# Kernel optimization log

Measured on AMD Instinct MI355X. Metric: run time of the kernel, lower is better.

Reference implementation:

```python
import math
import jax, jax.numpy as jnp
import numpy as np

B, T, C = 2, 2048, 1024
H, Ca = 16, 64


def setup_inputs() -> dict:
    key = jax.random.key(0)
    ks = jax.random.split(key, 5)
    # kaiming-uniform-ish scale for weights
    wb = 1.0 / math.sqrt(C)
    return {
        "x": jax.random.normal(ks[0], (B, T, C), dtype=jnp.float32),
        "w_q": jax.random.uniform(ks[1], (H, C, Ca), jnp.float32, -wb, wb),
        "w_k": jax.random.uniform(ks[2], (H, C, Ca), jnp.float32, -wb, wb),
        "w_v": jax.random.uniform(ks[3], (H, C, Ca), jnp.float32, -wb, wb),
        "w_o": jax.random.uniform(ks[4], (C, C), jnp.float32, -wb, wb),
    }


def reference(x, w_q, w_k, w_v, w_o):
    # x: [B,T,C]; w_q/w_k/w_v: [H,C,Ca]; w_o: [C,C]
    scale = 1.0 / math.sqrt(w_q.shape[-1])
    q = jnp.einsum("btc,hca->bhta", x, w_q)  # [B,H,T,Ca]
    k = jnp.einsum("btc,hca->bhta", x, w_k)
    v = jnp.einsum("btc,hca->bhta", x, w_v)
    s = jnp.einsum("bhta,bhsa->bhts", q, k)  # [B,H,T,T]
    # faithful to original: mask where tril(s)==0, scale applied after masking
    s_hat = jnp.where(jnp.tril(s) == 0, -jnp.inf, s * scale)
    a = jax.nn.softmax(s_hat, axis=-1)
    y = jnp.einsum("bhts,bhsa->bhta", a, v)  # [B,H,T,Ca]
    y_cat = y.transpose(0, 2, 1, 3).reshape(x.shape)  # [B,T,C]
    return y_cat @ w_o
```

## Files before the change

### kernel.cpp

```cpp
#include <hip/hip_runtime.h>
#include <stdint.h>

#define Bc 2
#define Tc 2048
#define Cn 1024
#define Hc 16
#define CAc 64

typedef __attribute__((ext_vector_type(8))) short short8;
typedef __attribute__((ext_vector_type(4))) float f32x4;

#define QSCALE 0.18033688011112042f

__device__ __forceinline__ unsigned short f2bf(float f) {
    unsigned int u = __builtin_bit_cast(unsigned int, f);
    return (unsigned short)((u + 0x7fffu + ((u >> 16) & 1u)) >> 16);
}
__device__ __forceinline__ unsigned int pack_rne(float a, float b) {
    return (unsigned int)f2bf(a) | ((unsigned int)f2bf(b) << 16);
}
__device__ __forceinline__ unsigned int pack_trunc(float a, float b) {
    return __builtin_amdgcn_perm(__builtin_bit_cast(unsigned int, b),
                                 __builtin_bit_cast(unsigned int, a), 0x07060302u);
}

__device__ __forceinline__ void async_cp16(const unsigned short* g, unsigned short* l) {
    __builtin_amdgcn_global_load_lds(
        (const __attribute__((address_space(1))) unsigned int*)g,
        (__attribute__((address_space(3))) unsigned int*)l,
        16, 0, 0);
}

__device__ __forceinline__ int detect_bf16(const unsigned short* x) {
    int c = 0;
#pragma unroll
    for (int i = 0; i < 64; i++) {
        unsigned short u = x[i * 2];
        int e = (u >> 7) & 0xFF;
        c += (e >= 0x68 && e <= 0x90);
    }
    return c > 32;
}

__device__ __forceinline__ unsigned short ld_elem(const void* base, size_t off, int isbf) {
    return isbf ? ((const unsigned short*)base)[off] : f2bf(((const float*)base)[off]);
}

__global__ __launch_bounds__(256) void prep(
    const void* __restrict__ xin, unsigned short* __restrict__ xb,
    const void* __restrict__ wq, const void* __restrict__ wk,
    const void* __restrict__ wv, const void* __restrict__ wo,
    unsigned short* __restrict__ wT, unsigned short* __restrict__ woT)
{
    const int isbf = detect_bf16((const unsigned short*)xin);
    const int bx = blockIdx.x;
    if (bx < 4096) {
        if (isbf) return;
        int idx = (bx * 256 + threadIdx.x) * 4;
        const float* xf = (const float*)xin;
        float4 v = *(const float4*)(xf + idx);
        uint2 p;
        p.x = pack_rne(v.x, v.y);
        p.y = pack_rne(v.z, v.w);
        *(uint2*)(&xb[idx]) = p;
        return;
    }
    __shared__ unsigned short tile[32][33];
    const int t = threadIdx.x;
    const int tx = t & 31, ty = t >> 5;
    const void* src;
    unsigned short* dst;
    int R, Cw, r0, c0;
    if (bx < 7168) {
        int rem0 = bx - 4096;
        int g = rem0 >> 6;
        int rem = rem0 & 63;
        int ct = rem >> 1;
        int at = rem & 1;
        int proj = g >> 4, h = g & 15;
        const void* wsel = (proj == 0) ? wq : ((proj == 1) ? wk : wv);
        src = isbf ? (const void*)((const unsigned short*)wsel + (size_t)h * Cn * CAc)
                   : (const void*)((const float*)wsel + (size_t)h * Cn * CAc);
        dst = wT + (size_t)g * CAc * Cn;
        R = Cn; Cw = CAc; r0 = ct * 32; c0 = at * 32;
    } else {
        int rem = bx - 7168;
        src = wo; dst = woT;
        R = Cn; Cw = Cn;
        r0 = (rem >> 5) * 32; c0 = (rem & 31) * 32;
    }
#pragma unroll
    for (int j = 0; j < 4; j++)
        tile[ty + j * 8][tx] = ld_elem(src, (size_t)(r0 + ty + j * 8) * Cw + c0 + tx, isbf);
    __syncthreads();
#pragma unroll
    for (int j = 0; j < 4; j++)
        dst[(size_t)(c0 + ty + j * 8) * R + r0 + tx] = tile[tx][ty + j * 8];
}

__global__ __launch_bounds__(128, 2) void gemm_qkv(
    const void* __restrict__ xin,
    const unsigned short* __restrict__ xb,
    const unsigned short* __restrict__ Bt,
    unsigned short* __restrict__ o0,
    unsigned short* __restrict__ o1,
    unsigned short* __restrict__ o2)
{
    __shared__ alignas(16) unsigned short SH[4][128 * 32];
    const int tid = threadIdx.x;
    const int wave = tid >> 6, lane = tid & 63;
    const int l15 = lane & 15, quad = lane >> 4;
    const int mBase = blockIdx.y * 128, nBase = blockIdx.x * 128;
    const int mOff = wave * 64;

    const int isbf = detect_bf16((const unsigned short*)xin);
    const unsigned short* Amat = isbf ? (const unsigned short*)xin : xb;

    const int srow = lane >> 2;
    const int sgc  = (lane & 3) ^ (srow & 3);
    const int sw = (quad ^ (l15 & 3)) * 8;

    f32x4 acc[4][8];
#pragma unroll
    for (int i = 0; i < 4; i++)
#pragma unroll
        for (int j = 0; j < 8; j++)
            acc[i][j] = (f32x4){0.f, 0.f, 0.f, 0.f};

#pragma unroll
    for (int t = 0; t < 4; t++) {
        int rl = wave * 64 + t * 16;
        async_cp16(Amat + (size_t)(mBase + rl + srow) * Cn + sgc * 8, &SH[0][rl * 32]);
        async_cp16(Bt   + (size_t)(nBase + rl + srow) * Cn + sgc * 8, &SH[2][rl * 32]);
    }
    __syncthreads();

    for (int kk = 0; kk < 32; kk++) {
        const int cur = kk & 1;
        if (kk < 31) {
            const int k1 = (kk + 1) * 32;
#pragma unroll
            for (int t = 0; t < 4; t++) {
                int rl = wave * 64 + t * 16;
                async_cp16(Amat + (size_t)(mBase + rl + srow) * Cn + k1 + sgc * 8, &SH[1 - cur][rl * 32]);
                async_cp16(Bt   + (size_t)(nBase + rl + srow) * Cn + k1 + sgc * 8, &SH[3 - cur][rl * 32]);
            }
        }
        short8 af[4], bfr[8];
#pragma unroll
        for (int i = 0; i < 4; i++)
            af[i] = *(const short8*)(&SH[cur][(mOff + i * 16 + l15) * 32 + sw]);
#pragma unroll
        for (int j = 0; j < 8; j++)
            bfr[j] = *(const short8*)(&SH[2 + cur][(j * 16 + l15) * 32 + sw]);
#pragma unroll
        for (int i = 0; i < 4; i++)
#pragma unroll
            for (int j = 0; j < 8; j++)
                acc[i][j] = __builtin_amdgcn_mfma_f32_16x16x32_bf16(af[i], bfr[j], acc[i][j], 0, 0, 0);
        __syncthreads();
    }

    const int bb = mBase >> 11;
    if (nBase < 2048) {
        const float sc = (nBase < 1024) ? QSCALE : 1.0f;
        unsigned short* dst = (nBase < 1024) ? o0 : o1;
#pragma unroll
        for (int i = 0; i < 4; i++) {
            int m0 = mBase + mOff + i * 16 + quad * 4;
            int t0 = m0 & (Tc - 1);
#pragma unroll
            for (int j = 0; j < 8; j++) {
                int n = nBase + j * 16 + l15;
                int h = (n >> 6) & 15, a = n & 63;
                size_t base = ((size_t)(bb * Hc + h) * Tc + t0) * CAc + a;
#pragma unroll
                for (int r = 0; r < 4; r++)
                    dst[base + (size_t)r * CAc] = f2bf(acc[i][j][r] * sc);
            }
        }
    } else {
        unsigned short* Cl = &SH[0][0];
#pragma unroll
        for (int i = 0; i < 4; i++) {
            int c16 = wave * 8 + i * 2 + (quad >> 1);
            int p = quad & 1;
#pragma unroll
            for (int j = 0; j < 8; j++) {
                int nl = j * 16 + l15;
                int cs = c16 ^ (nl & 7);
                uint2 v8;
                v8.x = pack_rne(acc[i][j][0], acc[i][j][1]);
                v8.y = pack_rne(acc[i][j][2], acc[i][j][3]);
                *(uint2*)(&Cl[nl * 128 + cs * 8 + p * 4]) = v8;
            }
        }
        __syncthreads();
        const int tLoc = mBase & (Tc - 1);
#pragma unroll
        for (int pp = 0; pp < 16; pp++) {
            int vr = pp * 8 + wave * 4 + (lane >> 4);
            int cc = lane & 15;
            int cs = cc ^ (vr & 7);
            uint4 val = *(const uint4*)(&Cl[vr * 128 + cs * 8]);
            int n = nBase + vr;
            int hh = (n >> 6) & 15, a = n & 63;
            *(uint4*)(&o2[((size_t)(bb * Hc + hh) * CAc + a) * Tc + tLoc + cc * 8]) = val;
        }
    }
}

__global__ __launch_bounds__(256) void gemm_out(
    const unsigned short* __restrict__ Amat,
    const unsigned short* __restrict__ Bt,
    void* __restrict__ o0,
    const void* __restrict__ xin)
{
    __shared__ alignas(16) unsigned short Al[2][64 * 32];
    __shared__ alignas(16) unsigned short Bl[2][128 * 32];
    const int tid = threadIdx.x;
    const int wave = tid >> 6, lane = tid & 63;
    const int l15 = lane & 15, quad = lane >> 4;
    const int mBase = blockIdx.y * 64, nBase = blockIdx.x * 128;
    const int mOff = (wave & 1) * 32, nOff = (wave >> 1) * 64;

    const int isbf = detect_bf16((const unsigned short*)xin);

    const int srow = lane >> 2;
    const int sgc  = (lane & 3) ^ (srow & 3);
    const int sw = (quad ^ (l15 & 3)) * 8;

    f32x4 acc[2][4];
#pragma unroll
    for (int i = 0; i < 2; i++)
#pragma unroll
        for (int j = 0; j < 4; j++)
            acc[i][j] = (f32x4){0.f, 0.f, 0.f, 0.f};

    {
        int rlA = wave * 16;
        async_cp16(Amat + (size_t)(mBase + rlA + srow) * Cn + sgc * 8, &Al[0][rlA * 32]);
#pragma unroll
        for (int t = 0; t < 2; t++) {
            int rlB = wave * 32 + t * 16;
            async_cp16(Bt + (size_t)(nBase + rlB + srow) * Cn + sgc * 8, &Bl[0][rlB * 32]);
        }
    }
    __syncthreads();

    for (int kk = 0; kk < 32; kk++) {
        const int cur = kk & 1;
        if (kk < 31) {
            const int k1 = (kk + 1) * 32;
            int rlA = wave * 16;
            async_cp16(Amat + (size_t)(mBase + rlA + srow) * Cn + k1 + sgc * 8, &Al[1 - cur][rlA * 32]);
#pragma unroll
            for (int t = 0; t < 2; t++) {
                int rlB = wave * 32 + t * 16;
                async_cp16(Bt + (size_t)(nBase + rlB + srow) * Cn + k1 + sgc * 8, &Bl[1 - cur][rlB * 32]);
            }
        }
        short8 af[2], bfr[4];
#pragma unroll
        for (int i = 0; i < 2; i++)
            af[i] = *(const short8*)(&Al[cur][(mOff + i * 16 + l15) * 32 + sw]);
#pragma unroll
        for (int j = 0; j < 4; j++)
            bfr[j] = *(const short8*)(&Bl[cur][(nOff + j * 16 + l15) * 32 + sw]);
#pragma unroll
        for (int i = 0; i < 2; i++)
#pragma unroll
            for (int j = 0; j < 4; j++)
                acc[i][j] = __builtin_amdgcn_mfma_f32_16x16x32_bf16(af[i], bfr[j], acc[i][j], 0, 0, 0);
        __syncthreads();
    }

#pragma unroll
    for (int i = 0; i < 2; i++) {
        int m0 = mBase + mOff + i * 16 + quad * 4;
#pragma unroll
        for (int j = 0; j < 4; j++) {
            int n = nBase + nOff + j * 16 + l15;
            if (isbf) {
#pragma unroll
                for (int r = 0; r < 4; r++)
                    ((unsigned short*)o0)[(size_t)(m0 + r) * Cn + n] = f2bf(acc[i][j][r]);
            } else {
#pragma unroll
                for (int r = 0; r < 4; r++)
                    ((float*)o0)[(size_t)(m0 + r) * Cn + n] = acc[i][j][r];
            }
        }
    }
}

__global__ __launch_bounds__(256, 4) void attn_t(
    const unsigned short* __restrict__ q,
    const unsigned short* __restrict__ k,
    const unsigned short* __restrict__ vT,
    unsigned short* __restrict__ y)
{
    __shared__ alignas(16) unsigned short Kl[2][64 * 64];
    __shared__ alignas(16) unsigned short Vl[2][64 * 64];
    __shared__ alignas(16) unsigned short Pl[4][16 * 64];
    const int bx = blockIdx.x;
    const int qt = 31 - (bx >> 5);
    const int bh = bx & 31;
    const int h = bh & 15, b = bh >> 4;
    const int tid = threadIdx.x;
    const int wave = tid >> 6, lane = tid & 63;
    const int l15 = lane & 15, quad = lane >> 4;
    const int m0w = qt * 64 + wave * 16;
    const size_t bhoff = (size_t)(b * Hc + h);
    const unsigned short* qh = q + bhoff * Tc * CAc;
    const unsigned short* kh = k + bhoff * Tc * CAc;
    const unsigned short* vh = vT + bhoff * CAc * Tc;

    const int srow = (lane >> 3);
    const int sgc  = (lane & 7) ^ srow;
    const int h7 = l15 & 7;
    const int sw0 = ((quad ^ h7) << 3);
    const int sw1 = (((4 + quad) ^ h7) << 3);
    const int pw_m = 2 * h7;

    short8 qf[2];
#pragma unroll
    for (int s = 0; s < 2; s++)
        qf[s] = *(const short8*)(&qh[(size_t)(m0w + l15) * CAc + s * 32 + quad * 8]);

    f32x4 oacc[4], osum;
#pragma unroll
    for (int j2 = 0; j2 < 4; j2++) oacc[j2] = (f32x4){0.f, 0.f, 0.f, 0.f};
    osum = (f32x4){0.f, 0.f, 0.f, 0.f};

    const unsigned short ONE = 0x3F80;
    short8 ones;
#pragma unroll
    for (int i = 0; i < 8; i++) ones[i] = (short)ONE;

    unsigned short* Pw = &Pl[wave][0];

#pragma unroll
    for (int t = 0; t < 2; t++) {
        int rl = wave * 16 + t * 8;
        async_cp16(kh + (size_t)(rl + srow) * CAc + sgc * 8, &Kl[0][rl * 64]);
        async_cp16(vh + (size_t)(rl + srow) * Tc  + sgc * 8, &Vl[0][rl * 64]);
    }
    __syncthreads();

    for (int kt = 0; kt <= qt; kt++) {
        const int k0 = kt * 64;
        const int cur = kt & 1;
        if (kt < qt) {
            const unsigned short* kg = kh + (size_t)(k0 + 64) * CAc;
            const unsigned short* vg = vh + (k0 + 64);
#pragma unroll
            for (int t = 0; t < 2; t++) {
                int rl = wave * 16 + t * 8;
                async_cp16(kg + (size_t)(rl + srow) * CAc + sgc * 8, &Kl[1 - cur][rl * 64]);
                async_cp16(vg + (size_t)(rl + srow) * Tc  + sgc * 8, &Vl[1 - cur][rl * 64]);
            }
        }
        const unsigned short* Kc = Kl[cur];
        const unsigned short* Vc = Vl[cur];

        float sv[4][4];
        __builtin_amdgcn_s_setprio(1);
#pragma unroll
        for (int j = 0; j < 4; j++) {
            short8 kf0 = *(const short8*)(&Kc[(j * 16 + l15) * 64 + sw0]);
            short8 kf1 = *(const short8*)(&Kc[(j * 16 + l15) * 64 + sw1]);
            f32x4 z = (f32x4){0.f, 0.f, 0.f, 0.f};
            z = __builtin_amdgcn_mfma_f32_16x16x32_bf16(kf0, qf[0], z, 0, 0, 0);
            z = __builtin_amdgcn_mfma_f32_16x16x32_bf16(kf1, qf[1], z, 0, 0, 0);
#pragma unroll
            for (int r = 0; r < 4; r++) sv[j][r] = z[r];
        }
        __builtin_amdgcn_s_setprio(0);

        if (kt == qt) {
            int tg = m0w + l15;
#pragma unroll
            for (int j = 0; j < 4; j++)
#pragma unroll
                for (int r = 0; r < 4; r++) {
                    int sg = k0 + j * 16 + quad * 4 + r;
                    sv[j][r] = (sg <= tg) ? __builtin_amdgcn_exp2f(sv[j][r]) : 0.f;
                }
        } else {
#pragma unroll
            for (int j = 0; j < 4; j++)
#pragma unroll
                for (int r = 0; r < 4; r++)
                    sv[j][r] = __builtin_amdgcn_exp2f(sv[j][r]);
        }

        short8 pa[2];
#pragma unroll
        for (int j = 0; j < 4; j++) {
            uint2 v;
            v.x = pack_trunc(sv[j][0], sv[j][1]);
            v.y = pack_trunc(sv[j][2], sv[j][3]);
            *(uint2*)(&Pw[l15 * 64 + ((j * 4 + quad) ^ pw_m) * 4]) = v;
        }
#pragma unroll
        for (int c = 0; c < 2; c++)
            pa[c] = *(const short8*)(&Pw[l15 * 64 + ((c * 4 + quad) ^ h7) * 8]);

        __builtin_amdgcn_s_setprio(1);
#pragma unroll
        for (int c = 0; c < 2; c++) {
#pragma unroll
            for (int j2 = 0; j2 < 4; j2++) {
                short8 vb = *(const short8*)(&Vc[(j2 * 16 + l15) * 64 + (c ? sw1 : sw0)]);
                oacc[j2] = __builtin_amdgcn_mfma_f32_16x16x32_bf16(pa[c], vb, oacc[j2], 0, 0, 0);
            }
            osum = __builtin_amdgcn_mfma_f32_16x16x32_bf16(pa[c], ones, osum, 0, 0, 0);
        }
        __builtin_amdgcn_s_setprio(0);
        __syncthreads();
    }

    float ri[4];
#pragma unroll
    for (int r = 0; r < 4; r++) ri[r] = 1.0f / osum[r];
#pragma unroll
    for (int j2 = 0; j2 < 4; j2++) {
#pragma unroll
        for (int r = 0; r < 4; r++) {
            int t = m0w + quad * 4 + r;
            y[((size_t)b * Tc + t) * Cn + h * CAc + j2 * 16 + l15] = f2bf(oacc[j2][r] * ri[r]);
        }
    }
}

extern "C" void kernel_launch(void* const* d_in, const int* in_sizes, int n_in,
                              void* d_out, int out_size, void* d_ws, size_t ws_size,
                              hipStream_t stream) {
    const void* x  = d_in[0];
    const void* wq = d_in[1];
    const void* wk = d_in[2];
    const void* wv = d_in[3];
    const void* wo = d_in[4];
    char* ws = (char*)d_ws;
    unsigned short* wT  = (unsigned short*)(ws + ((size_t)1 << 20));
    unsigned short* woT = (unsigned short*)(ws + ((size_t)7 << 20));
    unsigned short* xb  = (unsigned short*)(ws + ((size_t)9 << 20));
    unsigned short* qb  = (unsigned short*)(ws + ((size_t)17 << 20));
    unsigned short* kb  = (unsigned short*)(ws + ((size_t)25 << 20));
    unsigned short* vTb = (unsigned short*)(ws + ((size_t)33 << 20));
    unsigned short* yb  = (unsigned short*)(ws + ((size_t)41 << 20));

    prep<<<dim3(8192), dim3(256), 0, stream>>>(x, xb, wq, wk, wv, wo, wT, woT);
    gemm_qkv<<<dim3(24, 32), dim3(128), 0, stream>>>(x, xb, wT, qb, kb, vTb);
    attn_t<<<dim3(1024), dim3(256), 0, stream>>>(qb, kb, vTb, yb);
    gemm_out<<<dim3(8, 64), dim3(256), 0, stream>>>(yb, woT, d_out, x);
}
```

Before: 186.5 us.

## Double query tile per attention block to reuse K/V tiles across two row groups

Each attention workgroup now handles 128 query rows instead of 64, with each wave owning two 16-row groups that share every K/V tile loaded into LDS. This halves K/V global traffic and the number of barrier-synchronized iterations per query row. In exchange, register pressure rises (launch bound lowered to 3 waves per SIMD), the grid shrinks to 512 blocks, and the diagonal blocks do more masked work. Causal load imbalance across blocks also grows.

Measured after the change: 225.2 us. 20.7% more time.

```diff
diff --git a/kernel.cpp b/kernel.cpp
--- a/kernel.cpp
+++ b/kernel.cpp
@@ -294,7 +294,7 @@
     }
 }
 
-__global__ __launch_bounds__(256, 4) void attn_t(
+__global__ __launch_bounds__(256, 3) void attn_t(
     const unsigned short* __restrict__ q,
     const unsigned short* __restrict__ k,
     const unsigned short* __restrict__ vT,
@@ -302,15 +302,15 @@
 {
     __shared__ alignas(16) unsigned short Kl[2][64 * 64];
     __shared__ alignas(16) unsigned short Vl[2][64 * 64];
-    __shared__ alignas(16) unsigned short Pl[4][16 * 64];
+    __shared__ alignas(16) unsigned short Pl[4][32 * 64];
     const int bx = blockIdx.x;
-    const int qt = 31 - (bx >> 5);
+    const int qt = 15 - (bx >> 5);
     const int bh = bx & 31;
     const int h = bh & 15, b = bh >> 4;
     const int tid = threadIdx.x;
     const int wave = tid >> 6, lane = tid & 63;
     const int l15 = lane & 15, quad = lane >> 4;
-    const int m0w = qt * 64 + wave * 16;
+    const int m0w = qt * 128 + wave * 32;
     const size_t bhoff = (size_t)(b * Hc + h);
     const unsigned short* qh = q + bhoff * Tc * CAc;
     const unsigned short* kh = k + bhoff * Tc * CAc;
@@ -323,15 +323,21 @@
     const int sw1 = (((4 + quad) ^ h7) << 3);
     const int pw_m = 2 * h7;
 
-    short8 qf[2];
-#pragma unroll
-    for (int s = 0; s < 2; s++)
-        qf[s] = *(const short8*)(&qh[(size_t)(m0w + l15) * CAc + s * 32 + quad * 8]);
-
-    f32x4 oacc[4], osum;
-#pragma unroll
-    for (int j2 = 0; j2 < 4; j2++) oacc[j2] = (f32x4){0.f, 0.f, 0.f, 0.f};
-    osum = (f32x4){0.f, 0.f, 0.f, 0.f};
+    short8 qf[2][2];
+#pragma unroll
+    for (int g = 0; g < 2; g++)
+#pragma unroll
+        for (int s = 0; s < 2; s++)
+            qf[g][s] = *(const short8*)(
+                &qh[(size_t)(m0w + g * 16 + l15) * CAc + s * 32 + quad * 8]);
+
+    f32x4 oacc[2][4], osum[2];
+#pragma unroll
+    for (int g = 0; g < 2; g++) {
+#pragma unroll
+        for (int j2 = 0; j2 < 4; j2++) oacc[g][j2] = (f32x4){0.f, 0.f, 0.f, 0.f};
+        osum[g] = (f32x4){0.f, 0.f, 0.f, 0.f};
+    }
 
     const unsigned short ONE = 0x3F80;
     short8 ones;
@@ -348,10 +354,11 @@
     }
     __syncthreads();
 
-    for (int kt = 0; kt <= qt; kt++) {
+    const int ktl = 2 * qt + 1;
+    for (int kt = 0; kt <= ktl; kt++) {
         const int k0 = kt * 64;
         const int cur = kt & 1;
-        if (kt < qt) {
+        if (kt < ktl) {
             const unsigned short* kg = kh + (size_t)(k0 + 64) * CAc;
             const unsigned short* vg = vh + (k0 + 64);
 #pragma unroll
@@ -364,48 +371,60 @@
         const unsigned short* Kc = Kl[cur];
         const unsigned short* Vc = Vl[cur];
 
-        float sv[4][4];
+        float sv[2][4][4];
         __builtin_amdgcn_s_setprio(1);
 #pragma unroll
         for (int j = 0; j < 4; j++) {
             short8 kf0 = *(const short8*)(&Kc[(j * 16 + l15) * 64 + sw0]);
             short8 kf1 = *(const short8*)(&Kc[(j * 16 + l15) * 64 + sw1]);
-            f32x4 z = (f32x4){0.f, 0.f, 0.f, 0.f};
-            z = __builtin_amdgcn_mfma_f32_16x16x32_bf16(kf0, qf[0], z, 0, 0, 0);
-            z = __builtin_amdgcn_mfma_f32_16x16x32_bf16(kf1, qf[1], z, 0, 0, 0);
-#pragma unroll
-            for (int r = 0; r < 4; r++) sv[j][r] = z[r];
+#pragma unroll
+            for (int g = 0; g < 2; g++) {
+                f32x4 z = (f32x4){0.f, 0.f, 0.f, 0.f};
+                z = __builtin_amdgcn_mfma_f32_16x16x32_bf16(kf0, qf[g][0], z, 0, 0, 0);
+                z = __builtin_amdgcn_mfma_f32_16x16x32_bf16(kf1, qf[g][1], z, 0, 0, 0);
+#pragma unroll
+                for (int r = 0; r < 4; r++) sv[g][j][r] = z[r];
+            }
         }
         __builtin_amdgcn_s_setprio(0);
 
-        if (kt == qt) {
-            int tg = m0w + l15;
-#pragma unroll
-            for (int j = 0; j < 4; j++)
-#pragma unroll
-                for (int r = 0; r < 4; r++) {
-                    int sg = k0 + j * 16 + quad * 4 + r;
-                    sv[j][r] = (sg <= tg) ? __builtin_amdgcn_exp2f(sv[j][r]) : 0.f;
-                }
+        if (kt >= 2 * qt) {
+#pragma unroll
+            for (int g = 0; g < 2; g++) {
+                int tg = m0w + g * 16 + l15;
+#pragma unroll
+                for (int j = 0; j < 4; j++)
+#pragma unroll
+                    for (int r = 0; r < 4; r++) {
+                        int sg = k0 + j * 16 + quad * 4 + r;
+                        sv[g][j][r] = (sg <= tg) ? __builtin_amdgcn_exp2f(sv[g][j][r]) : 0.f;
+                    }
+            }
         } else {
 #pragma unroll
-            for (int j = 0; j < 4; j++)
-#pragma unroll
-                for (int r = 0; r < 4; r++)
-                    sv[j][r] = __builtin_amdgcn_exp2f(sv[j][r]);
-        }
-
-        short8 pa[2];
-#pragma unroll
-        for (int j = 0; j < 4; j++) {
-            uint2 v;
-            v.x = pack_trunc(sv[j][0], sv[j][1]);
-            v.y = pack_trunc(sv[j][2], sv[j][3]);
-            *(uint2*)(&Pw[l15 * 64 + ((j * 4 + quad) ^ pw_m) * 4]) = v;
-        }
-#pragma unroll
-        for (int c = 0; c < 2; c++)
-            pa[c] = *(const short8*)(&Pw[l15 * 64 + ((c * 4 + quad) ^ h7) * 8]);
+            for (int g = 0; g < 2; g++)
+#pragma unroll
+                for (int j = 0; j < 4; j++)
+#pragma unroll
+                    for (int r = 0; r < 4; r++)
+                        sv[g][j][r] = __builtin_amdgcn_exp2f(sv[g][j][r]);
+        }
+
+        short8 pa[2][2];
+#pragma unroll
+        for (int g = 0; g < 2; g++)
+#pragma unroll
+            for (int j = 0; j < 4; j++) {
+                uint2 v;
+                v.x = pack_trunc(sv[g][j][0], sv[g][j][1]);
+                v.y = pack_trunc(sv[g][j][2], sv[g][j][3]);
+                *(uint2*)(&Pw[(g * 16 + l15) * 64 + ((j * 4 + quad) ^ pw_m) * 4]) = v;
+            }
+#pragma unroll
+        for (int g = 0; g < 2; g++)
+#pragma unroll
+            for (int c = 0; c < 2; c++)
+                pa[g][c] = *(const short8*)(&Pw[(g * 16 + l15) * 64 + ((c * 4 + quad) ^ h7) * 8]);
 
         __builtin_amdgcn_s_setprio(1);
 #pragma unroll
@@ -413,23 +432,30 @@
 #pragma unroll
             for (int j2 = 0; j2 < 4; j2++) {
                 short8 vb = *(const short8*)(&Vc[(j2 * 16 + l15) * 64 + (c ? sw1 : sw0)]);
-                oacc[j2] = __builtin_amdgcn_mfma_f32_16x16x32_bf16(pa[c], vb, oacc[j2], 0, 0, 0);
-            }
-            osum = __builtin_amdgcn_mfma_f32_16x16x32_bf16(pa[c], ones, osum, 0, 0, 0);
+#pragma unroll
+                for (int g = 0; g < 2; g++)
+                    oacc[g][j2] = __builtin_amdgcn_mfma_f32_16x16x32_bf16(pa[g][c], vb, oacc[g][j2], 0, 0, 0);
+            }
+#pragma unroll
+            for (int g = 0; g < 2; g++)
+                osum[g] = __builtin_amdgcn_mfma_f32_16x16x32_bf16(pa[g][c], ones, osum[g], 0, 0, 0);
         }
         __builtin_amdgcn_s_setprio(0);
         __syncthreads();
     }
 
-    float ri[4];
-#pragma unroll
-    for (int r = 0; r < 4; r++) ri[r] = 1.0f / osum[r];
-#pragma unroll
-    for (int j2 = 0; j2 < 4; j2++) {
-#pragma unroll
-        for (int r = 0; r < 4; r++) {
-            int t = m0w + quad * 4 + r;
-            y[((size_t)b * Tc + t) * Cn + h * CAc + j2 * 16 + l15] = f2bf(oacc[j2][r] * ri[r]);
+#pragma unroll
+    for (int g = 0; g < 2; g++) {
+        float ri[4];
+#pragma unroll
+        for (int r = 0; r < 4; r++) ri[r] = 1.0f / osum[g][r];
+#pragma unroll
+        for (int j2 = 0; j2 < 4; j2++) {
+#pragma unroll
+            for (int r = 0; r < 4; r++) {
+                int t = m0w + g * 16 + quad * 4 + r;
+                y[((size_t)b * Tc + t) * Cn + h * CAc + j2 * 16 + l15] = f2bf(oacc[g][j2][r] * ri[r]);
+            }
         }
     }
 }
@@ -453,6 +479,6 @@
 
     prep<<<dim3(8192), dim3(256), 0, stream>>>(x, xb, wq, wk, wv, wo, wT, woT);
     gemm_qkv<<<dim3(24, 32), dim3(128), 0, stream>>>(x, xb, wT, qb, kb, vTb);
-    attn_t<<<dim3(1024), dim3(256), 0, stream>>>(qb, kb, vTb, yb);
+    attn_t<<<dim3(512), dim3(256), 0, stream>>>(qb, kb, vTb, yb);
     gemm_out<<<dim3(8, 64), dim3(256), 0, stream>>>(yb, woT, d_out, x);
 }
```
